# Kernel optimization log

Measured on AMD Instinct MI355X. Metric: run time of the kernel, lower is better.

Reference implementation:

```python
import jax, jax.numpy as jnp
import numpy as np

NUM_HEADS = 8
EPS = 1e-12  # tf.nn.l2_normalize epsilon


def _l2_normalize(t):
    # tf.nn.l2_normalize: x * rsqrt(max(sum(x^2), eps)) along last axis
    sq = jnp.sum(t * t, axis=-1, keepdims=True)
    return t * jax.lax.rsqrt(jnp.maximum(sq, EPS))


def setup_inputs() -> dict:
    key = jax.random.key(0)
    ks = jax.random.split(key, 4)
    B, N, C = 8, 4096, 512
    x = jax.random.normal(ks[0], (B, N, C), dtype=jnp.float32)
    w_qkv = jax.random.normal(ks[1], (C, 3 * C), dtype=jnp.float32) * (C ** -0.5)
    b_qkv = jnp.zeros((3 * C,), dtype=jnp.float32)
    w_proj = jax.random.normal(ks[2], (C, C), dtype=jnp.float32) * (C ** -0.5)
    b_proj = jnp.zeros((C,), dtype=jnp.float32)
    return {"x": x, "w_qkv": w_qkv, "b_qkv": b_qkv, "w_proj": w_proj, "b_proj": b_proj}


def reference(x, w_qkv, b_qkv, w_proj, b_proj):
    B, N, C = x.shape
    h = NUM_HEADS
    d = C // h
    scale = d ** -0.5
    qkv = x @ w_qkv + b_qkv                        # [B,N,3C]
    qkv = qkv.reshape(B, N, 3, h, d)
    qkv = jnp.transpose(qkv, (2, 0, 3, 1, 4))      # [3,B,h,N,d]
    q, k, v = qkv[0], qkv[1], qkv[2]
    q = _l2_normalize(q) * scale
    k = _l2_normalize(k)
    # channel-wise attention: q^T k over tokens -> [B,h,d,d]
    attn = jnp.einsum('bhnd,bhne->bhde', q, k)
    attn = jax.nn.softmax(attn, axis=-1)
    out = jnp.einsum('bhnd,bhde->bhne', v, attn)   # [B,h,N,d]
    out = jnp.transpose(out, (0, 2, 1, 3)).reshape(B, N, C)
    out = out @ w_proj + b_proj
    return out
```

## Files before the change

kernel.cpp:

```cpp
#include <hip/hip_runtime.h>
#include <stdint.h>

#define NB 8
#define NN 4096
#define NC 512
#define NH 8
#define ATTN_CH 16

typedef __bf16 bf16x8 __attribute__((ext_vector_type(8)));
typedef float floatx4 __attribute__((ext_vector_type(4)));

__device__ __forceinline__ unsigned short f2bf(float f) {
  union { float f; unsigned u; } v; v.f = f;
  return (unsigned short)((v.u + 0x7fffu + ((v.u >> 16) & 1u)) >> 16);
}
__device__ __forceinline__ float2 bfp2f(unsigned u) {
  union { unsigned x; float f; } lo, hi;
  lo.x = u << 16; hi.x = u & 0xffff0000u;
  return make_float2(lo.f, hi.f);
}

__device__ __forceinline__ void async_ld16(void* lds, const void* g) {
  auto* gp = (const __attribute__((address_space(1))) unsigned int*)(uintptr_t)g;
  auto* lp = (__attribute__((address_space(3))) unsigned int*)(uintptr_t)lds;
  __builtin_amdgcn_global_load_lds(gp, lp, 16, 0, 0);
}

__global__ __launch_bounds__(256) void k_prep(const float* __restrict__ x,
                                              unsigned short* __restrict__ xb,
                                              const float* __restrict__ w,
                                              unsigned short* __restrict__ wt) {
  int bid = blockIdx.x;
  if (bid < 16384) {
    int i = (bid * 256 + threadIdx.x) * 4;
    float4 v = *(const float4*)(x + i);
    ushort4 o;
    o.x = f2bf(v.x); o.y = f2bf(v.y); o.z = f2bf(v.z); o.w = f2bf(v.w);
    *(ushort4*)(xb + i) = o;
    return;
  }
  __shared__ float tile[64][65];
  int b2 = bid - 16384;
  int nn0 = (b2 % 24) * 64, kk0 = (b2 / 24) * 64;
  int t = threadIdx.x;
#pragma unroll
  for (int i = 0; i < 16; i++) {
    int id = t + i * 256;
    int r = id >> 6, c = id & 63;
    tile[c][r] = w[(size_t)(kk0 + r) * 1536 + nn0 + c];
  }
  __syncthreads();
#pragma unroll
  for (int i = 0; i < 16; i++) {
    int id = t + i * 256;
    int rn = id >> 6, ck = id & 63;
    wt[(size_t)(nn0 + rn) * 512 + kk0 + ck] = f2bf(tile[rn][ck]);
  }
}

__global__ __launch_bounds__(256) void k_gemm_qkv(const unsigned short* __restrict__ A,
                                                  const unsigned short* __restrict__ Bt,
                                                  const float* __restrict__ bias,
                                                  unsigned short* __restrict__ Cq) {
  const int K = 512, LDA = 512, LDB = 512, LDC = 1536;
  int bid = blockIdx.x;
  int xcd = bid & 7, local = bid >> 3;
  int mloc = local / 12, nt = local - mloc * 12;
  int m0 = (xcd * 32 + mloc) * 128, n0 = nt * 128;

  int tid = threadIdx.x;
  int lane = tid & 63, w = tid >> 6;
  int wm = (w & 1) * 64, wn = (w >> 1) * 64;
  int quad = lane >> 4, rr = lane & 15;
  int r8 = lane >> 3, cg = lane & 7;
  int cgs = cg ^ r8;
  const int swz = rr & 7;

  __shared__ __align__(16) unsigned short Als[128][64];
  __shared__ __align__(16) unsigned short Bls[128][64];

  floatx4 acc[4][4];
#pragma unroll
  for (int i = 0; i < 4; i++)
#pragma unroll
    for (int j = 0; j < 4; j++) acc[i][j] = (floatx4){0.f, 0.f, 0.f, 0.f};

  for (int k0 = 0; k0 < K; k0 += 64) {
#pragma unroll
    for (int i = 0; i < 4; i++) {
      int row = i * 32 + w * 8 + r8;
      async_ld16(&Als[i * 32 + w * 8][0], A + (size_t)(m0 + row) * LDA + k0 + cgs * 8);
      async_ld16(&Bls[i * 32 + w * 8][0], Bt + (size_t)(n0 + row) * LDB + k0 + cgs * 8);
    }
    __syncthreads();
#pragma unroll
    for (int kk = 0; kk < 64; kk += 32) {
      int gb = kk >> 3;
      bf16x8 af[4], bfr[4];
#pragma unroll
      for (int mi = 0; mi < 4; mi++)
        af[mi] = *(const bf16x8*)&Als[wm + mi * 16 + rr][(((gb + quad) ^ swz)) * 8];
#pragma unroll
      for (int ni = 0; ni < 4; ni++)
        bfr[ni] = *(const bf16x8*)&Bls[wn + ni * 16 + rr][(((gb + quad) ^ swz)) * 8];
#pragma unroll
      for (int mi = 0; mi < 4; mi++)
#pragma unroll
        for (int ni = 0; ni < 4; ni++)
          acc[mi][ni] = __builtin_amdgcn_mfma_f32_16x16x32_bf16(af[mi], bfr[ni], acc[mi][ni], 0, 0, 0);
    }
    __syncthreads();
  }
#pragma unroll
  for (int ni = 0; ni < 4; ni++) {
    int col = n0 + wn + ni * 16 + rr;
    float bv = bias[col];
#pragma unroll
    for (int mi = 0; mi < 4; mi++) {
      int rbase = m0 + wm + mi * 16 + quad * 4;
#pragma unroll
      for (int r = 0; r < 4; r++)
        Cq[(size_t)(rbase + r) * LDC + col] = f2bf(acc[mi][ni][r] + bv);
    }
  }
}

__global__ __launch_bounds__(256) void k_attn(const unsigned short* __restrict__ QKV,
                                              float* __restrict__ logits_p) {
  int chunk = blockIdx.x, hh = blockIdx.y, b = blockIdx.z;
  int tid = threadIdx.x, w = tid >> 6, l = tid & 63;
  int quad = l >> 4, rr = l & 15;

  __shared__ __align__(16) unsigned char smem[40960];
  unsigned short* qT = (unsigned short*)smem + w * 5120;
  unsigned short* kT = qT + 2560;
  float* ps = (float*)smem;

  floatx4 acc[4][4];
#pragma unroll
  for (int i = 0; i < 4; i++)
#pragma unroll
    for (int j = 0; j < 4; j++) acc[i][j] = (floatx4){0.f, 0.f, 0.f, 0.f};

  int tok8 = l >> 3;
  int seg = l & 7;
  int sw = seg & 3;

  for (int s = 0; s < 2; s++) {
    int nbase = chunk * 256 + w * 64 + s * 32;
#pragma unroll
    for (int c = 0; c < 4; c++) {
      int n = nbase + c * 8 + tok8;
      const unsigned short* p = QKV + (size_t)(b * 4096 + n) * 1536 + hh * 64 + seg * 8;
      uint4 vq = *(const uint4*)p;
      uint4 vk = *(const uint4*)(p + 512);
      unsigned uq[4] = {vq.x, vq.y, vq.z, vq.w};
      unsigned uk[4] = {vk.x, vk.y, vk.z, vk.w};
      float qf[8], kf[8], sq = 0.f, sk = 0.f;
#pragma unroll
      for (int e = 0; e < 4; e++) {
        float2 f = bfp2f(uq[e]); qf[2 * e] = f.x; qf[2 * e + 1] = f.y; sq += f.x * f.x + f.y * f.y;
        float2 g = bfp2f(uk[e]); kf[2 * e] = g.x; kf[2 * e + 1] = g.y; sk += g.x * g.x + g.y * g.y;
      }
      sq += __shfl_xor(sq, 1); sq += __shfl_xor(sq, 2); sq += __shfl_xor(sq, 4);
      sk += __shfl_xor(sk, 1); sk += __shfl_xor(sk, 2); sk += __shfl_xor(sk, 4);
      float scq = 0.125f * rsqrtf(fmaxf(sq, 1e-12f));
      float sck = rsqrtf(fmaxf(sk, 1e-12f));
      int col = ((c ^ sw) << 3) + tok8;
#pragma unroll
      for (int j = 0; j < 8; j++) {
        int dim = seg * 8 + j;
        qT[dim * 40 + col] = f2bf(qf[j] * scq);
        kT[dim * 40 + col] = f2bf(kf[j] * sck);
      }
    }
    bf16x8 af[4], bfr[4];
#pragma unroll
    for (int mi = 0; mi < 4; mi++) {
      int s3 = (mi * 2 + (rr >> 3)) & 3;
      int off = (mi * 16 + rr) * 40 + ((quad ^ s3) << 3);
      af[mi] = *(const bf16x8*)(qT + off);
      bfr[mi] = *(const bf16x8*)(kT + off);
    }
#pragma unroll
    for (int mi = 0; mi < 4; mi++)
#pragma unroll
      for (int ni = 0; ni < 4; ni++)
        acc[mi][ni] = __builtin_amdgcn_mfma_f32_16x16x32_bf16(af[mi], bfr[ni], acc[mi][ni], 0, 0, 0);
  }

  __syncthreads();
  for (int r2 = 0; r2 < 4; r2++) {
    if (w == r2) {
#pragma unroll
      for (int mi = 0; mi < 4; mi++)
#pragma unroll
        for (int ni = 0; ni < 4; ni++)
#pragma unroll
          for (int r = 0; r < 4; r++) {
            int d = mi * 16 + quad * 4 + r, e = ni * 16 + rr;
            if (r2 == 0) ps[d * 64 + e] = acc[mi][ni][r];
            else         ps[d * 64 + e] += acc[mi][ni][r];
          }
    }
    __syncthreads();
  }
  float* outp = logits_p + ((size_t)(b * 8 + hh) * ATTN_CH + chunk) * 4096;
  for (int i = tid; i < 4096; i += 256) outp[i] = ps[i];
}

__global__ __launch_bounds__(256) void k_softmax_m(const float* __restrict__ logits_p,
                                                   const float* __restrict__ wproj,
                                                   unsigned short* __restrict__ Mt) {
  int cc = blockIdx.x & 3, rh = blockIdx.x >> 2;
  int hh = blockIdx.y, b = blockIdx.z;
  int t = threadIdx.x;
  __shared__ float ls[32][64];
  __shared__ float red[32][8];
  __shared__ float inv[32];
  const float* lp = logits_p + (size_t)((b * 8 + hh) * ATTN_CH) * 4096 + rh * 2048;
#pragma unroll
  for (int i = 0; i < 8; i++) {
    int id = t + i * 256;
    float s = 0.f;
#pragma unroll
    for (int c = 0; c < ATTN_CH; c++) s += lp[c * 4096 + id];
    ls[id >> 6][id & 63] = s;
  }
  __syncthreads();
  int row = t >> 3, part = t & 7;
  float mx = -1e30f;
#pragma unroll
  for (int j = 0; j < 8; j++) mx = fmaxf(mx, ls[row][part * 8 + j]);
  red[row][part] = mx;
  __syncthreads();
  if (part == 0) {
    float m2 = red[row][0];
#pragma unroll
    for (int j = 1; j < 8; j++) m2 = fmaxf(m2, red[row][j]);
    inv[row] = m2;
  }
  __syncthreads();
  float rm = inv[row];
  float s = 0.f;
#pragma unroll
  for (int j = 0; j < 8; j++) {
    float e = __expf(ls[row][part * 8 + j] - rm);
    ls[row][part * 8 + j] = e;
    s += e;
  }
  red[row][part] = s;
  __syncthreads();
  if (part == 0) {
    float s2 = 0.f;
#pragma unroll
    for (int j = 0; j < 8; j++) s2 += red[row][j];
    inv[row] = 1.0f / s2;
  }
  __syncthreads();

  int cout = cc * 128 + (t & 127);
  int half = t >> 7;
  float wreg[64];
#pragma unroll
  for (int ee = 0; ee < 64; ee++) wreg[ee] = wproj[(size_t)(hh * 64 + ee) * 512 + cout];
  unsigned short ob[16];
#pragma unroll
  for (int d2 = 0; d2 < 16; d2++) {
    int dd = half * 16 + d2;
    float a = 0.f;
#pragma unroll
    for (int e4 = 0; e4 < 16; e4++) {
      float4 p4 = *(const float4*)&ls[dd][e4 * 4];
      a += p4.x * wreg[e4 * 4] + p4.y * wreg[e4 * 4 + 1] + p4.z * wreg[e4 * 4 + 2] + p4.w * wreg[e4 * 4 + 3];
    }
    ob[d2] = f2bf(a * inv[dd]);
  }
  uint4* dst = (uint4*)(Mt + ((size_t)(b * 512 + cout)) * 512 + hh * 64 + rh * 32 + half * 16);
  dst[0] = ((const uint4*)ob)[0];
  dst[1] = ((const uint4*)ob)[1];
}

__global__ __launch_bounds__(256) void k_gemm_out(const unsigned short* __restrict__ QKV,
                                                  const unsigned short* __restrict__ MtAll,
                                                  const float* __restrict__ bias,
                                                  float* __restrict__ Out) {
  const int K = 512, LDA = 1536, LDB = 512, LDC = 512;
  int bid = blockIdx.x;
  int xcd = bid & 7, local = bid >> 3;
  int mloc = local >> 2, nt = local & 3;
  int g = xcd * 32 + mloc;
  int b = g >> 5;
  int m0 = (g & 31) * 128;
  int n0 = nt * 128;
  const unsigned short* A = QKV + (size_t)b * NN * 1536 + 1024;
  const unsigned short* Bt = MtAll + (size_t)b * 512 * 512;
  int tid = threadIdx.x;
  int lane = tid & 63, w = tid >> 6;
  int wm = (w & 1) * 64, wn = (w >> 1) * 64;
  int quad = lane >> 4, rr = lane & 15;
  int r8 = lane >> 3, cg = lane & 7;
  int cgs = cg ^ r8;
  const int swz = rr & 7;

  __shared__ __align__(16) unsigned short Als[128][64];
  __shared__ __align__(16) unsigned short Bls[128][64];

  floatx4 acc[4][4];
#pragma unroll
  for (int i = 0; i < 4; i++)
#pragma unroll
    for (int j = 0; j < 4; j++) acc[i][j] = (floatx4){0.f, 0.f, 0.f, 0.f};

  for (int k0 = 0; k0 < K; k0 += 64) {
#pragma unroll
    for (int i = 0; i < 4; i++) {
      int row = i * 32 + w * 8 + r8;
      async_ld16(&Als[i * 32 + w * 8][0], A + (size_t)(m0 + row) * LDA + k0 + cgs * 8);
      async_ld16(&Bls[i * 32 + w * 8][0], Bt + (size_t)(n0 + row) * LDB + k0 + cgs * 8);
    }
    __syncthreads();
#pragma unroll
    for (int kk = 0; kk < 64; kk += 32) {
      int gb = kk >> 3;
      bf16x8 af[4], bfr[4];
#pragma unroll
      for (int mi = 0; mi < 4; mi++)
        af[mi] = *(const bf16x8*)&Als[wm + mi * 16 + rr][(((gb + quad) ^ swz)) * 8];
#pragma unroll
      for (int ni = 0; ni < 4; ni++)
        bfr[ni] = *(const bf16x8*)&Bls[wn + ni * 16 + rr][(((gb + quad) ^ swz)) * 8];
#pragma unroll
      for (int mi = 0; mi < 4; mi++)
#pragma unroll
        for (int ni = 0; ni < 4; ni++)
          acc[mi][ni] = __builtin_amdgcn_mfma_f32_16x16x32_bf16(af[mi], bfr[ni], acc[mi][ni], 0, 0, 0);
    }
    __syncthreads();
  }
#pragma unroll
  for (int ni = 0; ni < 4; ni++) {
    int col = n0 + wn + ni * 16 + rr;
    float bv = bias[col];
#pragma unroll
    for (int mi = 0; mi < 4; mi++) {
      int rbase = m0 + wm + mi * 16 + quad * 4;
#pragma unroll
      for (int r = 0; r < 4; r++)
        Out[(size_t)b * NN * LDC + (size_t)(rbase + r) * LDC + col] = acc[mi][ni][r] + bv;
    }
  }
}

extern "C" void kernel_launch(void* const* d_in, const int* in_sizes, int n_in,
                              void* d_out, int out_size, void* d_ws, size_t ws_size,
                              hipStream_t stream) {
  const float* x      = (const float*)d_in[0];
  const float* w_qkv  = (const float*)d_in[1];
  const float* b_qkv  = (const float*)d_in[2];
  const float* w_proj = (const float*)d_in[3];
  const float* b_proj = (const float*)d_in[4];
  float* out = (float*)d_out;

  char* ws = (char*)d_ws;
  size_t off = 0;
  auto alloc = [&](size_t bytes) -> void* {
    void* p = ws + off;
    off += (bytes + 255) & ~(size_t)255;
    return p;
  };
  unsigned short* xb       = (unsigned short*)alloc((size_t)NB * NN * NC * 2);
  unsigned short* wT       = (unsigned short*)alloc((size_t)1536 * 512 * 2);
  unsigned short* qkvb     = (unsigned short*)alloc((size_t)NB * NN * 3 * NC * 2);
  float*          logits_p = (float*)alloc((size_t)NB * NH * ATTN_CH * 4096 * 4);
  unsigned short* Mt       = (unsigned short*)alloc((size_t)NB * 512 * 512 * 2);

  k_prep<<<16576, 256, 0, stream>>>(x, xb, w_qkv, wT);
  k_gemm_qkv<<<3072, 256, 0, stream>>>(xb, wT, b_qkv, qkvb);
  k_attn<<<dim3(ATTN_CH, 8, 8), 256, 0, stream>>>(qkvb, logits_p);
  k_softmax_m<<<dim3(8, 8, 8), 256, 0, stream>>>(logits_p, w_proj, Mt);
  k_gemm_out<<<1024, 256, 0, stream>>>(qkvb, Mt, b_proj, out);
}
```

Baseline: 266.8 us.

## Use 256x256 double-buffered async-load tiles with 512 threads for both GEMMs

```diff
diff --git a/kernel.cpp b/kernel.cpp
--- a/kernel.cpp
+++ b/kernel.cpp
@@ -58,66 +58,98 @@
   }
 }
 
-__global__ __launch_bounds__(256) void k_gemm_qkv(const unsigned short* __restrict__ A,
-                                                  const unsigned short* __restrict__ Bt,
-                                                  const float* __restrict__ bias,
-                                                  unsigned short* __restrict__ Cq) {
-  const int K = 512, LDA = 512, LDB = 512, LDC = 1536;
+__global__ __launch_bounds__(512, 2) void k_gemm_qkv(const unsigned short* __restrict__ A,
+                                                     const unsigned short* __restrict__ Bt,
+                                                     const float* __restrict__ bias,
+                                                     unsigned short* __restrict__ Cq) {
+  const int LDA = 512, LDB = 512, LDC = 1536;
   int bid = blockIdx.x;
   int xcd = bid & 7, local = bid >> 3;
-  int mloc = local / 12, nt = local - mloc * 12;
-  int m0 = (xcd * 32 + mloc) * 128, n0 = nt * 128;
+  int mloc = local / 6, nt = local - mloc * 6;
+  int m0 = (xcd * 16 + mloc) * 256, n0 = nt * 256;
 
   int tid = threadIdx.x;
   int lane = tid & 63, w = tid >> 6;
-  int wm = (w & 1) * 64, wn = (w >> 1) * 64;
+  int wrb = (w >> 2) * 128;
+  int wcb = (w & 3) * 64;
   int quad = lane >> 4, rr = lane & 15;
   int r8 = lane >> 3, cg = lane & 7;
-  int cgs = cg ^ r8;
+  int cgs8 = (cg ^ r8) * 8;
   const int swz = rr & 7;
-
-  __shared__ __align__(16) unsigned short Als[128][64];
-  __shared__ __align__(16) unsigned short Bls[128][64];
-
-  floatx4 acc[4][4];
-#pragma unroll
-  for (int i = 0; i < 4; i++)
+  int w8 = w * 8;
+
+  __shared__ __align__(16) unsigned short As[2][256 * 64];
+  __shared__ __align__(16) unsigned short Bs[2][256 * 64];
+
+  floatx4 acc[8][4];
+#pragma unroll
+  for (int i = 0; i < 8; i++)
 #pragma unroll
     for (int j = 0; j < 4; j++) acc[i][j] = (floatx4){0.f, 0.f, 0.f, 0.f};
 
-  for (int k0 = 0; k0 < K; k0 += 64) {
+  auto stage = [&](int ss, int kt) {
+    int k0 = kt << 6;
 #pragma unroll
     for (int i = 0; i < 4; i++) {
-      int row = i * 32 + w * 8 + r8;
-      async_ld16(&Als[i * 32 + w * 8][0], A + (size_t)(m0 + row) * LDA + k0 + cgs * 8);
-      async_ld16(&Bls[i * 32 + w * 8][0], Bt + (size_t)(n0 + row) * LDB + k0 + cgs * 8);
-    }
-    __syncthreads();
-#pragma unroll
-    for (int kk = 0; kk < 64; kk += 32) {
-      int gb = kk >> 3;
-      bf16x8 af[4], bfr[4];
-#pragma unroll
-      for (int mi = 0; mi < 4; mi++)
-        af[mi] = *(const bf16x8*)&Als[wm + mi * 16 + rr][(((gb + quad) ^ swz)) * 8];
-#pragma unroll
-      for (int ni = 0; ni < 4; ni++)
-        bfr[ni] = *(const bf16x8*)&Bls[wn + ni * 16 + rr][(((gb + quad) ^ swz)) * 8];
-#pragma unroll
-      for (int mi = 0; mi < 4; mi++)
-#pragma unroll
-        for (int ni = 0; ni < 4; ni++)
-          acc[mi][ni] = __builtin_amdgcn_mfma_f32_16x16x32_bf16(af[mi], bfr[ni], acc[mi][ni], 0, 0, 0);
-    }
-    __syncthreads();
-  }
+      int rb = i * 64 + w8;
+      async_ld16(&As[ss][rb * 64], A + (size_t)(m0 + rb + r8) * LDA + k0 + cgs8);
+      async_ld16(&Bs[ss][rb * 64], Bt + (size_t)(n0 + rb + r8) * LDB + k0 + cgs8);
+    }
+  };
+
+  auto compute = [&](int ss) {
+#pragma unroll
+    for (int kk = 0; kk < 2; kk++) {
+      int ksl = (((kk << 2) + quad) ^ swz) << 3;
+      bf16x8 af[8];
+#pragma unroll
+      for (int mi = 0; mi < 8; mi++)
+        af[mi] = *(const bf16x8*)&As[ss][(wrb + mi * 16 + rr) * 64 + ksl];
+      bf16x8 bf[2];
+#pragma unroll
+      for (int ni = 0; ni < 2; ni++)
+        bf[ni] = *(const bf16x8*)&Bs[ss][(wcb + ni * 16 + rr) * 64 + ksl];
+      __builtin_amdgcn_s_setprio(1);
+#pragma unroll
+      for (int mi = 0; mi < 8; mi++)
+#pragma unroll
+        for (int ni = 0; ni < 2; ni++)
+          acc[mi][ni] = __builtin_amdgcn_mfma_f32_16x16x32_bf16(af[mi], bf[ni], acc[mi][ni], 0, 0, 0);
+      __builtin_amdgcn_s_setprio(0);
+#pragma unroll
+      for (int ni = 0; ni < 2; ni++)
+        bf[ni] = *(const bf16x8*)&Bs[ss][(wcb + (ni + 2) * 16 + rr) * 64 + ksl];
+      __builtin_amdgcn_s_setprio(1);
+#pragma unroll
+      for (int mi = 0; mi < 8; mi++)
+#pragma unroll
+        for (int ni = 0; ni < 2; ni++)
+          acc[mi][ni + 2] = __builtin_amdgcn_mfma_f32_16x16x32_bf16(af[mi], bf[ni], acc[mi][ni + 2], 0, 0, 0);
+      __builtin_amdgcn_s_setprio(0);
+    }
+  };
+
+  stage(0, 0);
+  stage(1, 1);
+#pragma unroll 1
+  for (int t = 0; t < 8; t++) {
+    if (t < 7) asm volatile("s_waitcnt vmcnt(8)" ::: "memory");
+    else       asm volatile("s_waitcnt vmcnt(0)" ::: "memory");
+    __builtin_amdgcn_s_barrier();
+    __builtin_amdgcn_sched_barrier(0);
+    compute(t & 1);
+    __builtin_amdgcn_sched_barrier(0);
+    __builtin_amdgcn_s_barrier();
+    if (t < 6) stage(t & 1, t + 2);
+  }
+
 #pragma unroll
   for (int ni = 0; ni < 4; ni++) {
-    int col = n0 + wn + ni * 16 + rr;
+    int col = n0 + wcb + ni * 16 + rr;
     float bv = bias[col];
 #pragma unroll
-    for (int mi = 0; mi < 4; mi++) {
-      int rbase = m0 + wm + mi * 16 + quad * 4;
+    for (int mi = 0; mi < 8; mi++) {
+      int rbase = m0 + wrb + mi * 16 + quad * 4;
 #pragma unroll
       for (int r = 0; r < 4; r++)
         Cq[(size_t)(rbase + r) * LDC + col] = f2bf(acc[mi][ni][r] + bv);
@@ -281,70 +313,103 @@
   dst[1] = ((const uint4*)ob)[1];
 }
 
-__global__ __launch_bounds__(256) void k_gemm_out(const unsigned short* __restrict__ QKV,
-                                                  const unsigned short* __restrict__ MtAll,
-                                                  const float* __restrict__ bias,
-                                                  float* __restrict__ Out) {
-  const int K = 512, LDA = 1536, LDB = 512, LDC = 512;
+__global__ __launch_bounds__(512, 2) void k_gemm_out(const unsigned short* __restrict__ QKV,
+                                                     const unsigned short* __restrict__ MtAll,
+                                                     const float* __restrict__ bias,
+                                                     float* __restrict__ Out) {
+  const int LDA = 1536, LDB = 512, LDC = 512;
   int bid = blockIdx.x;
   int xcd = bid & 7, local = bid >> 3;
-  int mloc = local >> 2, nt = local & 3;
-  int g = xcd * 32 + mloc;
-  int b = g >> 5;
-  int m0 = (g & 31) * 128;
-  int n0 = nt * 128;
+  int gid = xcd * 32 + local;
+  int b = gid >> 5;
+  int id = gid & 31;
+  int m0 = (id >> 1) * 256;
+  int n0 = (id & 1) * 256;
   const unsigned short* A = QKV + (size_t)b * NN * 1536 + 1024;
   const unsigned short* Bt = MtAll + (size_t)b * 512 * 512;
+
   int tid = threadIdx.x;
   int lane = tid & 63, w = tid >> 6;
-  int wm = (w & 1) * 64, wn = (w >> 1) * 64;
+  int wrb = (w >> 2) * 128;
+  int wcb = (w & 3) * 64;
   int quad = lane >> 4, rr = lane & 15;
   int r8 = lane >> 3, cg = lane & 7;
-  int cgs = cg ^ r8;
+  int cgs8 = (cg ^ r8) * 8;
   const int swz = rr & 7;
-
-  __shared__ __align__(16) unsigned short Als[128][64];
-  __shared__ __align__(16) unsigned short Bls[128][64];
-
-  floatx4 acc[4][4];
-#pragma unroll
-  for (int i = 0; i < 4; i++)
+  int w8 = w * 8;
+
+  __shared__ __align__(16) unsigned short As[2][256 * 64];
+  __shared__ __align__(16) unsigned short Bs[2][256 * 64];
+
+  floatx4 acc[8][4];
+#pragma unroll
+  for (int i = 0; i < 8; i++)
 #pragma unroll
     for (int j = 0; j < 4; j++) acc[i][j] = (floatx4){0.f, 0.f, 0.f, 0.f};
 
-  for (int k0 = 0; k0 < K; k0 += 64) {
+  auto stage = [&](int ss, int kt) {
+    int k0 = kt << 6;
 #pragma unroll
     for (int i = 0; i < 4; i++) {
-      int row = i * 32 + w * 8 + r8;
-      async_ld16(&Als[i * 32 + w * 8][0], A + (size_t)(m0 + row) * LDA + k0 + cgs * 8);
-      async_ld16(&Bls[i * 32 + w * 8][0], Bt + (size_t)(n0 + row) * LDB + k0 + cgs * 8);
-    }
-    __syncthreads();
-#pragma unroll
-    for (int kk = 0; kk < 64; kk += 32) {
-      int gb = kk >> 3;
-      bf16x8 af[4], bfr[4];
-#pragma unroll
-      for (int mi = 0; mi < 4; mi++)
-        af[mi] = *(const bf16x8*)&Als[wm + mi * 16 + rr][(((gb + quad) ^ swz)) * 8];
-#pragma unroll
-      for (int ni = 0; ni < 4; ni++)
-        bfr[ni] = *(const bf16x8*)&Bls[wn + ni * 16 + rr][(((gb + quad) ^ swz)) * 8];
-#pragma unroll
-      for (int mi = 0; mi < 4; mi++)
-#pragma unroll
-        for (int ni = 0; ni < 4; ni++)
-          acc[mi][ni] = __builtin_amdgcn_mfma_f32_16x16x32_bf16(af[mi], bfr[ni], acc[mi][ni], 0, 0, 0);
-    }
-    __syncthreads();
-  }
+      int rb = i * 64 + w8;
+      async_ld16(&As[ss][rb * 64], A + (size_t)(m0 + rb + r8) * LDA + k0 + cgs8);
+      async_ld16(&Bs[ss][rb * 64], Bt + (size_t)(n0 + rb + r8) * LDB + k0 + cgs8);
+    }
+  };
+
+  auto compute = [&](int ss) {
+#pragma unroll
+    for (int kk = 0; kk < 2; kk++) {
+      int ksl = (((kk << 2) + quad) ^ swz) << 3;
+      bf16x8 af[8];
+#pragma unroll
+      for (int mi = 0; mi < 8; mi++)
+        af[mi] = *(const bf16x8*)&As[ss][(wrb + mi * 16 + rr) * 64 + ksl];
+      bf16x8 bf[2];
+#pragma unroll
+      for (int ni = 0; ni < 2; ni++)
+        bf[ni] = *(const bf16x8*)&Bs[ss][(wcb + ni * 16 + rr) * 64 + ksl];
+      __builtin_amdgcn_s_setprio(1);
+#pragma unroll
+      for (int mi = 0; mi < 8; mi++)
+#pragma unroll
+        for (int ni = 0; ni < 2; ni++)
+          acc[mi][ni] = __builtin_amdgcn_mfma_f32_16x16x32_bf16(af[mi], bf[ni], acc[mi][ni], 0, 0, 0);
+      __builtin_amdgcn_s_setprio(0);
+#pragma unroll
+      for (int ni = 0; ni < 2; ni++)
+        bf[ni] = *(const bf16x8*)&Bs[ss][(wcb + (ni + 2) * 16 + rr) * 64 + ksl];
+      __builtin_amdgcn_s_setprio(1);
+#pragma unroll
+      for (int mi = 0; mi < 8; mi++)
+#pragma unroll
+        for (int ni = 0; ni < 2; ni++)
+          acc[mi][ni + 2] = __builtin_amdgcn_mfma_f32_16x16x32_bf16(af[mi], bf[ni], acc[mi][ni + 2], 0, 0, 0);
+      __builtin_amdgcn_s_setprio(0);
+    }
+  };
+
+  stage(0, 0);
+  stage(1, 1);
+#pragma unroll 1
+  for (int t = 0; t < 8; t++) {
+    if (t < 7) asm volatile("s_waitcnt vmcnt(8)" ::: "memory");
+    else       asm volatile("s_waitcnt vmcnt(0)" ::: "memory");
+    __builtin_amdgcn_s_barrier();
+    __builtin_amdgcn_sched_barrier(0);
+    compute(t & 1);
+    __builtin_amdgcn_sched_barrier(0);
+    __builtin_amdgcn_s_barrier();
+    if (t < 6) stage(t & 1, t + 2);
+  }
+
 #pragma unroll
   for (int ni = 0; ni < 4; ni++) {
-    int col = n0 + wn + ni * 16 + rr;
+    int col = n0 + wcb + ni * 16 + rr;
     float bv = bias[col];
 #pragma unroll
-    for (int mi = 0; mi < 4; mi++) {
-      int rbase = m0 + wm + mi * 16 + quad * 4;
+    for (int mi = 0; mi < 8; mi++) {
+      int rbase = m0 + wrb + mi * 16 + quad * 4;
 #pragma unroll
       for (int r = 0; r < 4; r++)
         Out[(size_t)b * NN * LDC + (size_t)(rbase + r) * LDC + col] = acc[mi][ni][r] + bv;
@@ -376,8 +441,8 @@
   unsigned short* Mt       = (unsigned short*)alloc((size_t)NB * 512 * 512 * 2);
 
   k_prep<<<16576, 256, 0, stream>>>(x, xb, w_qkv, wT);
-  k_gemm_qkv<<<3072, 256, 0, stream>>>(xb, wT, b_qkv, qkvb);
+  k_gemm_qkv<<<768, 512, 0, stream>>>(xb, wT, b_qkv, qkvb);
   k_attn<<<dim3(ATTN_CH, 8, 8), 256, 0, stream>>>(qkvb, logits_p);
   k_softmax_m<<<dim3(8, 8, 8), 256, 0, stream>>>(logits_p, w_proj, Mt);
-  k_gemm_out<<<1024, 256, 0, stream>>>(qkvb, Mt, b_proj, out);
-}
+  k_gemm_out<<<256, 512, 0, stream>>>(qkvb, Mt, b_proj, out);
+}
```

Result: slower. 287.5 us (+7.8%).

## Software-pipeline QKV and output GEMMs with multi-stage async LDS buffers

Applied to the files above, without the earlier changes.

```diff
diff --git a/kernel.cpp b/kernel.cpp
--- a/kernel.cpp
+++ b/kernel.cpp
@@ -58,11 +58,11 @@
   }
 }
 
-__global__ __launch_bounds__(256) void k_gemm_qkv(const unsigned short* __restrict__ A,
-                                                  const unsigned short* __restrict__ Bt,
-                                                  const float* __restrict__ bias,
-                                                  unsigned short* __restrict__ Cq) {
-  const int K = 512, LDA = 512, LDB = 512, LDC = 1536;
+__global__ __launch_bounds__(256, 2) void k_gemm_qkv(const unsigned short* __restrict__ A,
+                                                     const unsigned short* __restrict__ Bt,
+                                                     const float* __restrict__ bias,
+                                                     unsigned short* __restrict__ Cq) {
+  const int LDA = 512, LDB = 512, LDC = 1536;
   int bid = blockIdx.x;
   int xcd = bid & 7, local = bid >> 3;
   int mloc = local / 12, nt = local - mloc * 12;
@@ -73,11 +73,11 @@
   int wm = (w & 1) * 64, wn = (w >> 1) * 64;
   int quad = lane >> 4, rr = lane & 15;
   int r8 = lane >> 3, cg = lane & 7;
-  int cgs = cg ^ r8;
+  int cgs8 = (cg ^ r8) * 8;
   const int swz = rr & 7;
 
-  __shared__ __align__(16) unsigned short Als[128][64];
-  __shared__ __align__(16) unsigned short Bls[128][64];
+  __shared__ __align__(16) unsigned short Als[3][128 * 64];
+  __shared__ __align__(16) unsigned short Bls[2][128 * 64];
 
   floatx4 acc[4][4];
 #pragma unroll
@@ -85,32 +85,55 @@
 #pragma unroll
     for (int j = 0; j < 4; j++) acc[i][j] = (floatx4){0.f, 0.f, 0.f, 0.f};
 
-  for (int k0 = 0; k0 < K; k0 += 64) {
+  auto stageA = [&](int ss, int kt) {
+    int k0 = kt << 6;
 #pragma unroll
     for (int i = 0; i < 4; i++) {
-      int row = i * 32 + w * 8 + r8;
-      async_ld16(&Als[i * 32 + w * 8][0], A + (size_t)(m0 + row) * LDA + k0 + cgs * 8);
-      async_ld16(&Bls[i * 32 + w * 8][0], Bt + (size_t)(n0 + row) * LDB + k0 + cgs * 8);
-    }
-    __syncthreads();
-#pragma unroll
-    for (int kk = 0; kk < 64; kk += 32) {
-      int gb = kk >> 3;
-      bf16x8 af[4], bfr[4];
-#pragma unroll
-      for (int mi = 0; mi < 4; mi++)
-        af[mi] = *(const bf16x8*)&Als[wm + mi * 16 + rr][(((gb + quad) ^ swz)) * 8];
+      int rb = i * 32 + w * 8;
+      async_ld16(&Als[ss][rb * 64], A + (size_t)(m0 + rb + r8) * LDA + k0 + cgs8);
+    }
+  };
+  auto stageB = [&](int ss, int kt) {
+    int k0 = kt << 6;
+#pragma unroll
+    for (int i = 0; i < 4; i++) {
+      int rb = i * 32 + w * 8;
+      async_ld16(&Bls[ss][rb * 64], Bt + (size_t)(n0 + rb + r8) * LDB + k0 + cgs8);
+    }
+  };
+
+  auto computeK = [&](int sa, int sb, int gb) {
+    bf16x8 af[4], bfr[4];
+#pragma unroll
+    for (int mi = 0; mi < 4; mi++)
+      af[mi] = *(const bf16x8*)&Als[sa][(wm + mi * 16 + rr) * 64 + (((gb + quad) ^ swz)) * 8];
+#pragma unroll
+    for (int ni = 0; ni < 4; ni++)
+      bfr[ni] = *(const bf16x8*)&Bls[sb][(wn + ni * 16 + rr) * 64 + (((gb + quad) ^ swz)) * 8];
+    __builtin_amdgcn_s_setprio(1);
+#pragma unroll
+    for (int mi = 0; mi < 4; mi++)
 #pragma unroll
       for (int ni = 0; ni < 4; ni++)
-        bfr[ni] = *(const bf16x8*)&Bls[wn + ni * 16 + rr][(((gb + quad) ^ swz)) * 8];
-#pragma unroll
-      for (int mi = 0; mi < 4; mi++)
-#pragma unroll
-        for (int ni = 0; ni < 4; ni++)
-          acc[mi][ni] = __builtin_amdgcn_mfma_f32_16x16x32_bf16(af[mi], bfr[ni], acc[mi][ni], 0, 0, 0);
-    }
-    __syncthreads();
-  }
+        acc[mi][ni] = __builtin_amdgcn_mfma_f32_16x16x32_bf16(af[mi], bfr[ni], acc[mi][ni], 0, 0, 0);
+    __builtin_amdgcn_s_setprio(0);
+  };
+
+  stageB(0, 0); stageA(0, 0); stageA(1, 1);
+  int sa = 0;
+#pragma unroll 1
+  for (int t = 0; t < 8; t++) {
+    if (t < 7) asm volatile("s_waitcnt vmcnt(4)" ::: "memory");
+    else       asm volatile("s_waitcnt vmcnt(0)" ::: "memory");
+    asm volatile("s_barrier" ::: "memory");
+    if (t < 7) stageB((t + 1) & 1, t + 1);
+    if (t < 6) { int s2 = sa + 2; if (s2 >= 3) s2 -= 3; stageA(s2, t + 2); }
+    __builtin_amdgcn_sched_barrier(0);
+    computeK(sa, t & 1, 0);
+    computeK(sa, t & 1, 4);
+    sa = (sa + 1 < 3) ? sa + 1 : 0;
+  }
+
 #pragma unroll
   for (int ni = 0; ni < 4; ni++) {
     int col = n0 + wn + ni * 16 + rr;
@@ -281,11 +304,11 @@
   dst[1] = ((const uint4*)ob)[1];
 }
 
-__global__ __launch_bounds__(256) void k_gemm_out(const unsigned short* __restrict__ QKV,
-                                                  const unsigned short* __restrict__ MtAll,
-                                                  const float* __restrict__ bias,
-                                                  float* __restrict__ Out) {
-  const int K = 512, LDA = 1536, LDB = 512, LDC = 512;
+__global__ __launch_bounds__(256, 2) void k_gemm_out(const unsigned short* __restrict__ QKV,
+                                                     const unsigned short* __restrict__ MtAll,
+                                                     const float* __restrict__ bias,
+                                                     float* __restrict__ Out) {
+  const int LDA = 1536, LDB = 512, LDC = 512;
   int bid = blockIdx.x;
   int xcd = bid & 7, local = bid >> 3;
   int mloc = local >> 2, nt = local & 3;
@@ -300,11 +323,11 @@
   int wm = (w & 1) * 64, wn = (w >> 1) * 64;
   int quad = lane >> 4, rr = lane & 15;
   int r8 = lane >> 3, cg = lane & 7;
-  int cgs = cg ^ r8;
+  int cgs8 = (cg ^ r8) * 8;
   const int swz = rr & 7;
 
-  __shared__ __align__(16) unsigned short Als[128][64];
-  __shared__ __align__(16) unsigned short Bls[128][64];
+  __shared__ __align__(16) unsigned short Als[3][128 * 64];
+  __shared__ __align__(16) unsigned short Bls[2][128 * 64];
 
   floatx4 acc[4][4];
 #pragma unroll
@@ -312,32 +335,55 @@
 #pragma unroll
     for (int j = 0; j < 4; j++) acc[i][j] = (floatx4){0.f, 0.f, 0.f, 0.f};
 
-  for (int k0 = 0; k0 < K; k0 += 64) {
+  auto stageA = [&](int ss, int kt) {
+    int k0 = kt << 6;
 #pragma unroll
     for (int i = 0; i < 4; i++) {
-      int row = i * 32 + w * 8 + r8;
-      async_ld16(&Als[i * 32 + w * 8][0], A + (size_t)(m0 + row) * LDA + k0 + cgs * 8);
-      async_ld16(&Bls[i * 32 + w * 8][0], Bt + (size_t)(n0 + row) * LDB + k0 + cgs * 8);
-    }
-    __syncthreads();
-#pragma unroll
-    for (int kk = 0; kk < 64; kk += 32) {
-      int gb = kk >> 3;
-      bf16x8 af[4], bfr[4];
-#pragma unroll
-      for (int mi = 0; mi < 4; mi++)
-        af[mi] = *(const bf16x8*)&Als[wm + mi * 16 + rr][(((gb + quad) ^ swz)) * 8];
+      int rb = i * 32 + w * 8;
+      async_ld16(&Als[ss][rb * 64], A + (size_t)(m0 + rb + r8) * LDA + k0 + cgs8);
+    }
+  };
+  auto stageB = [&](int ss, int kt) {
+    int k0 = kt << 6;
+#pragma unroll
+    for (int i = 0; i < 4; i++) {
+      int rb = i * 32 + w * 8;
+      async_ld16(&Bls[ss][rb * 64], Bt + (size_t)(n0 + rb + r8) * LDB + k0 + cgs8);
+    }
+  };
+
+  auto computeK = [&](int sa, int sb, int gb) {
+    bf16x8 af[4], bfr[4];
+#pragma unroll
+    for (int mi = 0; mi < 4; mi++)
+      af[mi] = *(const bf16x8*)&Als[sa][(wm + mi * 16 + rr) * 64 + (((gb + quad) ^ swz)) * 8];
+#pragma unroll
+    for (int ni = 0; ni < 4; ni++)
+      bfr[ni] = *(const bf16x8*)&Bls[sb][(wn + ni * 16 + rr) * 64 + (((gb + quad) ^ swz)) * 8];
+    __builtin_amdgcn_s_setprio(1);
+#pragma unroll
+    for (int mi = 0; mi < 4; mi++)
 #pragma unroll
       for (int ni = 0; ni < 4; ni++)
-        bfr[ni] = *(const bf16x8*)&Bls[wn + ni * 16 + rr][(((gb + quad) ^ swz)) * 8];
-#pragma unroll
-      for (int mi = 0; mi < 4; mi++)
-#pragma unroll
-        for (int ni = 0; ni < 4; ni++)
-          acc[mi][ni] = __builtin_amdgcn_mfma_f32_16x16x32_bf16(af[mi], bfr[ni], acc[mi][ni], 0, 0, 0);
-    }
-    __syncthreads();
-  }
+        acc[mi][ni] = __builtin_amdgcn_mfma_f32_16x16x32_bf16(af[mi], bfr[ni], acc[mi][ni], 0, 0, 0);
+    __builtin_amdgcn_s_setprio(0);
+  };
+
+  stageB(0, 0); stageA(0, 0); stageA(1, 1);
+  int sa = 0;
+#pragma unroll 1
+  for (int t = 0; t < 8; t++) {
+    if (t < 7) asm volatile("s_waitcnt vmcnt(4)" ::: "memory");
+    else       asm volatile("s_waitcnt vmcnt(0)" ::: "memory");
+    asm volatile("s_barrier" ::: "memory");
+    if (t < 7) stageB((t + 1) & 1, t + 1);
+    if (t < 6) { int s2 = sa + 2; if (s2 >= 3) s2 -= 3; stageA(s2, t + 2); }
+    __builtin_amdgcn_sched_barrier(0);
+    computeK(sa, t & 1, 0);
+    computeK(sa, t & 1, 4);
+    sa = (sa + 1 < 3) ? sa + 1 : 0;
+  }
+
 #pragma unroll
   for (int ni = 0; ni < 4; ni++) {
     int col = n0 + wn + ni * 16 + rr;
```

New measurement: 260.4 us. 1.02x faster.
